# Kernel optimization log

Measured on AMD Instinct MI355X. Metric: run time of the kernel, lower is better.

The kernel has to match this reference:

```python
import jax, jax.numpy as jnp
import numpy as np

TEMPERATURE = 1.0
MAX_ITERS = 10
EPSILON = 1e-4
N, D, K = 131072, 64, 64


def setup_inputs() -> dict:
    key = jax.random.key(0)
    k1, k2 = jax.random.split(key)
    weights = jax.random.normal(k1, (N, D), dtype=jnp.float32)
    init_clusters = jax.random.normal(k2, (K, D), dtype=jnp.float32)
    return {"weights": weights, "init_clusters": init_clusters}


def _dkm(weights, init_clusters):
    n, d = weights.shape
    k = init_clusters.shape[0]
    w_sq = jnp.sum(weights * weights, axis=1, keepdims=True)  # [N,1]

    def step(carry, _):
        clusters, attn_prev, done = carry
        # Euclidean cdist via the expansion ||w||^2 + ||c||^2 - 2 w.c
        c_sq = jnp.sum(clusters * clusters, axis=1)               # [K]
        d2 = w_sq + c_sq[None, :] - 2.0 * (weights @ clusters.T)  # [N,K]
        dist = jnp.sqrt(jnp.maximum(d2, 0.0))
        attn = jax.nn.softmax(-dist / TEMPERATURE, axis=-1)        # [N,K]
        new_clusters = (attn.T @ weights) / jnp.sum(attn, axis=0)[:, None]  # [K,D]
        converged = jnp.linalg.norm(clusters - new_clusters) <= EPSILON
        # Torch breaks BEFORE assigning new_clusters; emulate with a done flag.
        clusters_next = jnp.where(done | converged, clusters, new_clusters)
        attn_next = jnp.where(done, attn_prev, attn)
        return (clusters_next, attn_next, done | converged), None

    init = (init_clusters, jnp.zeros((n, k), weights.dtype), jnp.array(False))
    (clusters, attn, _), _ = jax.lax.scan(step, init, None, length=MAX_ITERS)
    compressed = attn @ clusters  # [N,D]
    return compressed, clusters, attn


def reference(weights, init_clusters):
    return _dkm(weights, init_clusters)
```

## Files before the change

kernel.cpp:

```cpp
#include <hip/hip_runtime.h>
#include <math.h>
#include <stdint.h>

#define N_ROWS 131072
#define DIM 64
#define KC 64
#define NBLK 1024
#define ROWS_PB 128

typedef __attribute__((ext_vector_type(8))) short short8;
typedef __attribute__((ext_vector_type(8))) unsigned short ushort8;
typedef __attribute__((ext_vector_type(16))) float float16;
typedef __attribute__((ext_vector_type(4))) unsigned int uint4v;
typedef __attribute__((ext_vector_type(2))) unsigned long long ulong2v;

#define PARTIAL_OFF 0u
#define SUMA_OFF    4194304u
#define NEWC_OFF    4259840u
#define NORM_BYTE_OFF (4263936ull * 4ull)

__device__ __forceinline__ uint32_t rne16(float a) {
  uint32_t u = __float_as_uint(a);
  return (u + 0x7fffu + ((u >> 16) & 1u)) >> 16;
}

__device__ __forceinline__ uint32_t pack_bf16(float a, float b) {
  return rne16(a) | (rne16(b) << 16);
}

__device__ __forceinline__ void split2(float a, float b, uint32_t& hi, uint32_t& lo) {
  uint32_t ha = rne16(a), hb = rne16(b);
  hi = ha | (hb << 16);
  float la = a - __uint_as_float(ha << 16);
  float lb = b - __uint_as_float(hb << 16);
  lo = pack_bf16(la, lb);
}

__global__ __launch_bounds__(256, 3) void dkm_iter(
    const float* __restrict__ W, const float* __restrict__ Cinit,
    const float* __restrict__ newC, float* __restrict__ cur,
    const double* __restrict__ normpart,
    float* __restrict__ partial, float* __restrict__ sumA,
    float* __restrict__ attn_out, int useSel, int writeAttn)
{
  __shared__ __align__(16) short CbfHi[64][68];
  __shared__ __align__(16) short CbfLo[64][68];
  __shared__ __align__(16) short attnT[64][136];
  __shared__ __align__(16) short WTsh[64][136];
  __shared__ float csqL[64];
  __shared__ float wsqL[128];
  __shared__ int s_cond;

  const int t = threadIdx.x;
  const int blk = blockIdx.x;
  const int wid = t >> 6, lane = t & 63, l31 = lane & 31, lh = lane >> 5;
  const int mg = wid >> 1, ng = wid & 1;
  const int chunkBase = blk * ROWS_PB;
  const int myrow = chunkBase + wid * 32 + l31;
  const int colA = wid * 32 + l31;

  if (wid == 0) {
    double v = 0.0;
    if (useSel) {
#pragma unroll
      for (int i = 0; i < 8; ++i) v += normpart[lane + 64 * i];
    }
    v += __shfl_xor(v, 1); v += __shfl_xor(v, 2); v += __shfl_xor(v, 4);
    v += __shfl_xor(v, 8); v += __shfl_xor(v, 16); v += __shfl_xor(v, 32);
    if (lane == 0) s_cond = (v > 1.0e-8) ? 1 : 0;
  }
  __syncthreads();

  const float* src = useSel ? (s_cond ? newC : cur) : Cinit;

  {
    const int crow = t >> 2, cc = (t & 3) * 16;
    float sq = 0.f;
#pragma unroll
    for (int q = 0; q < 4; ++q) {
      float4 c0 = *(const float4*)(src + crow * 64 + cc + q * 4);
      if (blk == 0) *(float4*)(cur + crow * 64 + cc + q * 4) = c0;
      uint32_t h0, h1, l0, l1;
      split2(c0.x, c0.y, h0, l0);
      split2(c0.z, c0.w, h1, l1);
      uint32_t* ph = (uint32_t*)&CbfHi[crow][cc + q * 4];
      ph[0] = h0; ph[1] = h1;
      uint32_t* pl = (uint32_t*)&CbfLo[crow][cc + q * 4];
      pl[0] = l0; pl[1] = l1;
      sq += c0.x*c0.x + c0.y*c0.y + c0.z*c0.z + c0.w*c0.w;
    }
    sq += __shfl_xor(sq, 1);
    sq += __shfl_xor(sq, 2);
    if ((t & 3) == 0) csqL[crow] = sq;
  }
  __syncthreads();

  float16 dot0 = {0,0,0,0, 0,0,0,0, 0,0,0,0, 0,0,0,0};
  float16 dot1 = {0,0,0,0, 0,0,0,0, 0,0,0,0, 0,0,0,0};
  float w2acc = 0.f;
  const float* pw = W + (size_t)myrow * 64 + lh * 8;
#pragma unroll
  for (int ko = 0; ko < 4; ++ko) {
    float4 a = *(const float4*)(pw + ko * 16);
    float4 b = *(const float4*)(pw + ko * 16 + 4);
    w2acc += a.x*a.x + a.y*a.y + a.z*a.z + a.w*a.w
           + b.x*b.x + b.y*b.y + b.z*b.z + b.w*b.w;
    uint32_t h0, h1, h2, h3, l0, l1, l2, l3;
    split2(a.x, a.y, h0, l0); split2(a.z, a.w, h1, l1);
    split2(b.x, b.y, h2, l2); split2(b.z, b.w, h3, l3);
    const int d0 = ko * 16 + lh * 8;
    WTsh[d0 + 0][colA] = (short)h0;  WTsh[d0 + 1][colA] = (short)(h0 >> 16);
    WTsh[d0 + 2][colA] = (short)h1;  WTsh[d0 + 3][colA] = (short)(h1 >> 16);
    WTsh[d0 + 4][colA] = (short)h2;  WTsh[d0 + 5][colA] = (short)(h2 >> 16);
    WTsh[d0 + 6][colA] = (short)h3;  WTsh[d0 + 7][colA] = (short)(h3 >> 16);
    uint4v th = {h0, h1, h2, h3};
    uint4v tl = {l0, l1, l2, l3};
    short8 aHi = __builtin_bit_cast(short8, th);
    short8 aLo = __builtin_bit_cast(short8, tl);
#pragma unroll
    for (int nt = 0; nt < 2; ++nt) {
      const unsigned long long* ph = (const unsigned long long*)&CbfHi[nt * 32 + l31][ko * 16 + lh * 8];
      const unsigned long long* pl = (const unsigned long long*)&CbfLo[nt * 32 + l31][ko * 16 + lh * 8];
      ulong2v vh = {ph[0], ph[1]};
      ulong2v vl = {pl[0], pl[1]};
      short8 cHi = __builtin_bit_cast(short8, vh);
      short8 cLo = __builtin_bit_cast(short8, vl);
      float16& dd = nt ? dot1 : dot0;
      dd = __builtin_amdgcn_mfma_f32_32x32x16_bf16(aHi, cHi, dd, 0, 0, 0);
      dd = __builtin_amdgcn_mfma_f32_32x32x16_bf16(aLo, cHi, dd, 0, 0, 0);
      dd = __builtin_amdgcn_mfma_f32_32x32x16_bf16(aHi, cLo, dd, 0, 0, 0);
    }
  }
  w2acc += __shfl_xor(w2acc, 32);
  if (lane < 32) wsqL[wid * 32 + l31] = w2acc;

  const float cq0 = csqL[l31], cq1 = csqL[32 + l31];
#pragma unroll
  for (int j = 0; j < 16; ++j) {
    const int trow = (j & 3) + 8 * (j >> 2) + 4 * lh;
    const float w2 = wsqL[wid * 32 + trow];
    float g0 = -sqrtf(fmaxf(fmaf(-2.f, dot0[j], w2 + cq0), 0.f));
    float g1 = -sqrtf(fmaxf(fmaf(-2.f, dot1[j], w2 + cq1), 0.f));
    dot0[j] = __expf(g0);
    dot1[j] = __expf(g1);
  }

  if (writeAttn) {
#pragma unroll
    for (int j = 0; j < 16; ++j) {
      const int trow = (j & 3) + 8 * (j >> 2) + 4 * lh;
      float sj = dot0[j] + dot1[j];
      sj += __shfl_xor(sj, 1);  sj += __shfl_xor(sj, 2);  sj += __shfl_xor(sj, 4);
      sj += __shfl_xor(sj, 8);  sj += __shfl_xor(sj, 16);
      float inv = __builtin_amdgcn_rcpf(sj);
      attn_out[(size_t)(chunkBase + wid * 32 + trow) * 64 + l31] = dot0[j] * inv;
      attn_out[(size_t)(chunkBase + wid * 32 + trow) * 64 + 32 + l31] = dot1[j] * inv;
    }
  }

  {
    uint32_t* aT = (uint32_t*)&attnT[0][0];
    const int cb = wid * 16;
#pragma unroll
    for (int h = 0; h < 4; ++h) {
      const int base = cb + 4 * h + 2 * lh;
      aT[l31 * 68 + base]     = pack_bf16(dot0[4 * h],     dot0[4 * h + 1]);
      aT[l31 * 68 + base + 1] = pack_bf16(dot0[4 * h + 2], dot0[4 * h + 3]);
      aT[(32 + l31) * 68 + base]     = pack_bf16(dot1[4 * h],     dot1[4 * h + 1]);
      aT[(32 + l31) * 68 + base + 1] = pack_bf16(dot1[4 * h + 2], dot1[4 * h + 3]);
    }
  }
  __syncthreads();

  float* invsL = wsqL;
  {
    const int r = t >> 1, kh = t & 1;
    float s = 0.f;
#pragma unroll
    for (int kk = 0; kk < 32; ++kk) {
      uint32_t v = (uint32_t)(unsigned short)attnT[kh * 32 + kk][r];
      s += __uint_as_float(v << 16);
    }
    s += __shfl_xor(s, 1);
    if (kh == 0) invsL[r] = __builtin_amdgcn_rcpf(s);
  }
  __syncthreads();

  {
    const int k = t >> 2, q = t & 3;
    uint32_t* row = (uint32_t*)&attnT[k][0];
#pragma unroll
    for (int i = 0; i < 16; ++i) {
      const int r2 = q * 32 + 2 * i;
      uint32_t dv = row[q * 16 + i];
      float lo = __uint_as_float(dv << 16) * invsL[r2];
      float hi = __uint_as_float(dv & 0xffff0000u) * invsL[r2 + 1];
      row[q * 16 + i] = pack_bf16(lo, hi);
    }
  }
  __syncthreads();

  float16 Uacc = {0,0,0,0, 0,0,0,0, 0,0,0,0, 0,0,0,0};
#pragma unroll
  for (int kc = 0; kc < 8; ++kc) {
    const unsigned long long* pa =
        (const unsigned long long*)&attnT[mg * 32 + l31][kc * 16 + lh * 8];
    ulong2v va = {pa[0], pa[1]};
    short8 af = __builtin_bit_cast(short8, va);
    const unsigned long long* pb =
        (const unsigned long long*)&WTsh[ng * 32 + l31][kc * 16 + lh * 8];
    ulong2v vb = {pb[0], pb[1]};
    short8 bf = __builtin_bit_cast(short8, vb);
    Uacc = __builtin_amdgcn_mfma_f32_32x32x16_bf16(af, bf, Uacc, 0, 0, 0);
  }

  float ssum = 0.f;
  {
    const int sk = t & 63, sg = t >> 6;
#pragma unroll
    for (int q2 = 0; q2 < 4; ++q2) {
      const uint32_t* pq = (const uint32_t*)&attnT[sk][sg * 32 + q2 * 8];
#pragma unroll
      for (int w = 0; w < 4; ++w) {
        uint32_t dv = pq[w];
        ssum += __uint_as_float(dv << 16) + __uint_as_float(dv & 0xffff0000u);
      }
    }
  }

#pragma unroll
  for (int j = 0; j < 16; ++j) {
    const int k = mg * 32 + (j & 3) + 8 * (j >> 2) + 4 * lh;
    partial[((size_t)blk * 64 + k) * 64 + ng * 32 + l31] = Uacc[j];
  }

  __syncthreads();
  float* red = (float*)&CbfHi[0][0];
  red[t] = ssum;
  __syncthreads();
  if (t < 64) sumA[blk * 64 + t] = (red[t] + red[t + 64]) + (red[t + 128] + red[t + 192]);
}

__global__ __launch_bounds__(256) void reduce_kernel(
    const float* __restrict__ partial, const float* __restrict__ sumAp,
    const float* __restrict__ curC, float* __restrict__ newC,
    double* __restrict__ normpart) {
  const int k = blockIdx.x >> 3, oct = blockIdx.x & 7;
  const int t = threadIdx.x;
  const int d = oct * 8 + (t & 7), q = t >> 3;
  double acc = 0.0;
  for (int b = q * 32; b < q * 32 + 32; ++b)
    acc += (double)partial[((size_t)b * 64 + k) * 64 + d];
  __shared__ double sh[256];
  __shared__ double sh2[256];
  sh[t] = acc;
  sh2[t] = ((double)sumAp[t * 64 + k] + (double)sumAp[(t + 256) * 64 + k]) +
           ((double)sumAp[(t + 512) * 64 + k] + (double)sumAp[(t + 768) * 64 + k]);
  __syncthreads();
#pragma unroll
  for (int s = 128; s >= 8; s >>= 1) {
    if (t < s) { sh[t] += sh[t + s]; sh2[t] += sh2[t + s]; }
    __syncthreads();
  }
#pragma unroll
  for (int s = 4; s >= 1; s >>= 1) {
    if (t < s) sh2[t] += sh2[t + s];
    __syncthreads();
  }
  if (t < 8) {
    float nc = (float)(sh[t] / sh2[0]);
    newC[k * 64 + d] = nc;
    double diff = (double)curC[k * 64 + d] - (double)nc;
    sh[t] = diff * diff;
  }
  __syncthreads();
  if (t == 0) {
    double s = 0.0;
#pragma unroll
    for (int i = 0; i < 8; ++i) s += sh[i];
    normpart[blockIdx.x] = s;
  }
}

__global__ __launch_bounds__(256) void finalize_kernel(
    const double* __restrict__ np, const float* __restrict__ newC,
    const float* __restrict__ cur, float* __restrict__ clusters_out) {
  __shared__ double sh[64];
  __shared__ int sc;
  int t = threadIdx.x;
  if (t < 64) {
    double v = 0.0;
#pragma unroll
    for (int i = 0; i < 8; ++i) v += np[t + 64 * i];
    sh[t] = v;
  }
  __syncthreads();
  if (t == 0) {
    double s = 0.0;
    for (int i = 0; i < 64; ++i) s += sh[i];
    sc = (s > 1.0e-8) ? 1 : 0;
  }
  __syncthreads();
  const float* src = sc ? newC : cur;
  for (int m = t; m < 4096; m += 256) {
    float v = src[m];
    clusters_out[m] = v;
  }
}

__global__ __launch_bounds__(256) void compress_kernel(
    const float* __restrict__ attn, const float* __restrict__ Cl,
    float* __restrict__ outC) {
  __shared__ float Csh[64 * 64];
  __shared__ float Ash[64 * 64];
  float4* Csh4 = (float4*)Csh;
  float4* Ash4 = (float4*)Ash;
  const int t = threadIdx.x;
  const int blk = blockIdx.x;
  const int rowBase = blk * 256;
  const int rg = t >> 4, dg = t & 15;

  {
    const float4* gC = (const float4*)Cl;
#pragma unroll
    for (int q = 0; q < 4; ++q) {
      int m = t + 256 * q;
      Csh4[m ^ ((m >> 6) & 15)] = gC[m];
    }
  }

  for (int tile = 0; tile < 4; ++tile) {
    __syncthreads();
    {
      const float4* gA = (const float4*)(attn + (size_t)(rowBase + tile * 64) * KC);
#pragma unroll
      for (int q = 0; q < 4; ++q) {
        int m = t + 256 * q;
        Ash4[m ^ ((m >> 6) & 15)] = gA[m];
      }
    }
    __syncthreads();
    float acc[4][4] = {{0.f}};
#pragma unroll 4
    for (int c = 0; c < 16; ++c) {
      float4 av[4], cv[4];
#pragma unroll
      for (int i = 0; i < 4; ++i) av[i] = Ash4[((rg * 4 + i) * 16 + c) ^ rg];
#pragma unroll
      for (int j = 0; j < 4; ++j) cv[j] = Csh4[((c * 4 + j) * 16 + dg) ^ c];
#pragma unroll
      for (int i = 0; i < 4; ++i) {
        float a0 = fmaf(av[i].x, cv[0].x, acc[i][0]);
        a0 = fmaf(av[i].y, cv[1].x, a0);
        a0 = fmaf(av[i].z, cv[2].x, a0);
        acc[i][0] = fmaf(av[i].w, cv[3].x, a0);
        float a1 = fmaf(av[i].x, cv[0].y, acc[i][1]);
        a1 = fmaf(av[i].y, cv[1].y, a1);
        a1 = fmaf(av[i].z, cv[2].y, a1);
        acc[i][1] = fmaf(av[i].w, cv[3].y, a1);
        float a2 = fmaf(av[i].x, cv[0].z, acc[i][2]);
        a2 = fmaf(av[i].y, cv[1].z, a2);
        a2 = fmaf(av[i].z, cv[2].z, a2);
        acc[i][2] = fmaf(av[i].w, cv[3].z, a2);
        float a3 = fmaf(av[i].x, cv[0].w, acc[i][3]);
        a3 = fmaf(av[i].y, cv[1].w, a3);
        a3 = fmaf(av[i].z, cv[2].w, a3);
        acc[i][3] = fmaf(av[i].w, cv[3].w, a3);
      }
    }
    float4* gO = (float4*)(outC + (size_t)(rowBase + tile * 64) * DIM);
#pragma unroll
    for (int i = 0; i < 4; ++i)
      gO[(rg * 4 + i) * 16 + dg] = make_float4(acc[i][0], acc[i][1], acc[i][2], acc[i][3]);
  }
}

extern "C" void kernel_launch(void* const* d_in, const int* in_sizes, int n_in,
                              void* d_out, int out_size, void* d_ws, size_t ws_size,
                              hipStream_t stream) {
  (void)in_sizes; (void)n_in; (void)d_ws; (void)ws_size; (void)out_size;
  const float* W = (const float*)d_in[0];
  const float* Cinit = (const float*)d_in[1];
  float* ob = (float*)d_out;

  float* compressed = ob;
  float* clusters_out = ob + (size_t)N_ROWS * DIM;
  float* attn_out = ob + (size_t)N_ROWS * DIM + KC * DIM;

  float* partial = ob + PARTIAL_OFF;
  float* sumAp = ob + SUMA_OFF;
  float* newC = ob + NEWC_OFF;
  float* cur = clusters_out;
  double* normpart = (double*)((char*)d_out + NORM_BYTE_OFF);

  for (int it = 0; it < 10; ++it) {
    dkm_iter<<<NBLK, 256, 0, stream>>>(W, Cinit, newC, cur, normpart,
                                       partial, sumAp, attn_out,
                                       (it > 0) ? 1 : 0, (it == 9) ? 1 : 0);
    reduce_kernel<<<512, 256, 0, stream>>>(partial, sumAp, cur, newC, normpart);
  }
  finalize_kernel<<<1, 256, 0, stream>>>(normpart, newC, cur, clusters_out);
  compress_kernel<<<512, 256, 0, stream>>>(attn_out, clusters_out, compressed);
}
```

Baseline: 375.6 us.

## Process two row chunks per block with register prefetch of next chunk's weights

Each block now handles 256 rows as two 128-row chunks, halving the block count and the per-block centroid setup and partial outputs. The weights for the second chunk are loaded into registers during the first chunk's distance/softmax work, so global loads overlap compute. The reduce kernel reads half as many partials, and the LDS normalisation loop staggers its index by row to reduce bank conflicts. The cost is higher register pressure from the prefetched float4 array and fewer blocks to fill the GPU (512 blocks).

```diff
diff --git a/kernel.cpp b/kernel.cpp
--- a/kernel.cpp
+++ b/kernel.cpp
@@ -5,8 +5,8 @@
 #define N_ROWS 131072
 #define DIM 64
 #define KC 64
-#define NBLK 1024
-#define ROWS_PB 128
+#define NBLK 512
+#define ROWS_PB 256
 
 typedef __attribute__((ext_vector_type(8))) short short8;
 typedef __attribute__((ext_vector_type(8))) unsigned short ushort8;
@@ -15,9 +15,9 @@
 typedef __attribute__((ext_vector_type(2))) unsigned long long ulong2v;
 
 #define PARTIAL_OFF 0u
-#define SUMA_OFF    4194304u
-#define NEWC_OFF    4259840u
-#define NORM_BYTE_OFF (4263936ull * 4ull)
+#define SUMA_OFF    2097152u
+#define NEWC_OFF    2129920u
+#define NORM_BYTE_OFF (2134016ull * 4ull)
 
 __device__ __forceinline__ uint32_t rne16(float a) {
   uint32_t u = __float_as_uint(a);
@@ -55,9 +55,14 @@
   const int blk = blockIdx.x;
   const int wid = t >> 6, lane = t & 63, l31 = lane & 31, lh = lane >> 5;
   const int mg = wid >> 1, ng = wid & 1;
-  const int chunkBase = blk * ROWS_PB;
-  const int myrow = chunkBase + wid * 32 + l31;
+  const int rowBase = blk * ROWS_PB;
   const int colA = wid * 32 + l31;
+
+  const float* pwBase = W + (size_t)(rowBase + wid * 32 + l31) * 64 + lh * 8;
+  float4 vv[8];
+#pragma unroll
+  for (int q = 0; q < 8; ++q)
+    vv[q] = *(const float4*)(pwBase + (q >> 1) * 16 + (q & 1) * 4);
 
   if (wid == 0) {
     double v = 0.0;
@@ -95,137 +100,151 @@
   }
   __syncthreads();
 
-  float16 dot0 = {0,0,0,0, 0,0,0,0, 0,0,0,0, 0,0,0,0};
-  float16 dot1 = {0,0,0,0, 0,0,0,0, 0,0,0,0, 0,0,0,0};
-  float w2acc = 0.f;
-  const float* pw = W + (size_t)myrow * 64 + lh * 8;
-#pragma unroll
-  for (int ko = 0; ko < 4; ++ko) {
-    float4 a = *(const float4*)(pw + ko * 16);
-    float4 b = *(const float4*)(pw + ko * 16 + 4);
-    w2acc += a.x*a.x + a.y*a.y + a.z*a.z + a.w*a.w
-           + b.x*b.x + b.y*b.y + b.z*b.z + b.w*b.w;
-    uint32_t h0, h1, h2, h3, l0, l1, l2, l3;
-    split2(a.x, a.y, h0, l0); split2(a.z, a.w, h1, l1);
-    split2(b.x, b.y, h2, l2); split2(b.z, b.w, h3, l3);
-    const int d0 = ko * 16 + lh * 8;
-    WTsh[d0 + 0][colA] = (short)h0;  WTsh[d0 + 1][colA] = (short)(h0 >> 16);
-    WTsh[d0 + 2][colA] = (short)h1;  WTsh[d0 + 3][colA] = (short)(h1 >> 16);
-    WTsh[d0 + 4][colA] = (short)h2;  WTsh[d0 + 5][colA] = (short)(h2 >> 16);
-    WTsh[d0 + 6][colA] = (short)h3;  WTsh[d0 + 7][colA] = (short)(h3 >> 16);
-    uint4v th = {h0, h1, h2, h3};
-    uint4v tl = {l0, l1, l2, l3};
-    short8 aHi = __builtin_bit_cast(short8, th);
-    short8 aLo = __builtin_bit_cast(short8, tl);
-#pragma unroll
-    for (int nt = 0; nt < 2; ++nt) {
-      const unsigned long long* ph = (const unsigned long long*)&CbfHi[nt * 32 + l31][ko * 16 + lh * 8];
-      const unsigned long long* pl = (const unsigned long long*)&CbfLo[nt * 32 + l31][ko * 16 + lh * 8];
-      ulong2v vh = {ph[0], ph[1]};
-      ulong2v vl = {pl[0], pl[1]};
-      short8 cHi = __builtin_bit_cast(short8, vh);
-      short8 cLo = __builtin_bit_cast(short8, vl);
-      float16& dd = nt ? dot1 : dot0;
-      dd = __builtin_amdgcn_mfma_f32_32x32x16_bf16(aHi, cHi, dd, 0, 0, 0);
-      dd = __builtin_amdgcn_mfma_f32_32x32x16_bf16(aLo, cHi, dd, 0, 0, 0);
-      dd = __builtin_amdgcn_mfma_f32_32x32x16_bf16(aHi, cLo, dd, 0, 0, 0);
-    }
-  }
-  w2acc += __shfl_xor(w2acc, 32);
-  if (lane < 32) wsqL[wid * 32 + l31] = w2acc;
-
+  float16 Uacc = {0,0,0,0, 0,0,0,0, 0,0,0,0, 0,0,0,0};
+  float ssumAll = 0.f;
   const float cq0 = csqL[l31], cq1 = csqL[32 + l31];
-#pragma unroll
-  for (int j = 0; j < 16; ++j) {
-    const int trow = (j & 3) + 8 * (j >> 2) + 4 * lh;
-    const float w2 = wsqL[wid * 32 + trow];
-    float g0 = -sqrtf(fmaxf(fmaf(-2.f, dot0[j], w2 + cq0), 0.f));
-    float g1 = -sqrtf(fmaxf(fmaf(-2.f, dot1[j], w2 + cq1), 0.f));
-    dot0[j] = __expf(g0);
-    dot1[j] = __expf(g1);
-  }
-
-  if (writeAttn) {
+
+#pragma unroll
+  for (int c = 0; c < 2; ++c) {
+    const int chunkBase = rowBase + c * 128;
+
+    float16 dot0 = {0,0,0,0, 0,0,0,0, 0,0,0,0, 0,0,0,0};
+    float16 dot1 = {0,0,0,0, 0,0,0,0, 0,0,0,0, 0,0,0,0};
+    float w2acc = 0.f;
+#pragma unroll
+    for (int ko = 0; ko < 4; ++ko) {
+      float4 a = vv[ko * 2];
+      float4 b = vv[ko * 2 + 1];
+      w2acc += a.x*a.x + a.y*a.y + a.z*a.z + a.w*a.w
+             + b.x*b.x + b.y*b.y + b.z*b.z + b.w*b.w;
+      uint32_t h0, h1, h2, h3, l0, l1, l2, l3;
+      split2(a.x, a.y, h0, l0); split2(a.z, a.w, h1, l1);
+      split2(b.x, b.y, h2, l2); split2(b.z, b.w, h3, l3);
+      const int d0 = ko * 16 + lh * 8;
+      WTsh[d0 + 0][colA] = (short)h0;  WTsh[d0 + 1][colA] = (short)(h0 >> 16);
+      WTsh[d0 + 2][colA] = (short)h1;  WTsh[d0 + 3][colA] = (short)(h1 >> 16);
+      WTsh[d0 + 4][colA] = (short)h2;  WTsh[d0 + 5][colA] = (short)(h2 >> 16);
+      WTsh[d0 + 6][colA] = (short)h3;  WTsh[d0 + 7][colA] = (short)(h3 >> 16);
+      uint4v th = {h0, h1, h2, h3};
+      uint4v tl = {l0, l1, l2, l3};
+      short8 aHi = __builtin_bit_cast(short8, th);
+      short8 aLo = __builtin_bit_cast(short8, tl);
+#pragma unroll
+      for (int nt = 0; nt < 2; ++nt) {
+        const unsigned long long* ph = (const unsigned long long*)&CbfHi[nt * 32 + l31][ko * 16 + lh * 8];
+        const unsigned long long* pl = (const unsigned long long*)&CbfLo[nt * 32 + l31][ko * 16 + lh * 8];
+        ulong2v vh = {ph[0], ph[1]};
+        ulong2v vl = {pl[0], pl[1]};
+        short8 cHi = __builtin_bit_cast(short8, vh);
+        short8 cLo = __builtin_bit_cast(short8, vl);
+        float16& dd = nt ? dot1 : dot0;
+        dd = __builtin_amdgcn_mfma_f32_32x32x16_bf16(aHi, cHi, dd, 0, 0, 0);
+        dd = __builtin_amdgcn_mfma_f32_32x32x16_bf16(aLo, cHi, dd, 0, 0, 0);
+        dd = __builtin_amdgcn_mfma_f32_32x32x16_bf16(aHi, cLo, dd, 0, 0, 0);
+      }
+    }
+    w2acc += __shfl_xor(w2acc, 32);
+    if (lane < 32) wsqL[wid * 32 + l31] = w2acc;
+
+    if (c == 0) {
+      const float* pwN = pwBase + 128 * 64;
+#pragma unroll
+      for (int q = 0; q < 8; ++q)
+        vv[q] = *(const float4*)(pwN + (q >> 1) * 16 + (q & 1) * 4);
+    }
+
 #pragma unroll
     for (int j = 0; j < 16; ++j) {
       const int trow = (j & 3) + 8 * (j >> 2) + 4 * lh;
-      float sj = dot0[j] + dot1[j];
-      sj += __shfl_xor(sj, 1);  sj += __shfl_xor(sj, 2);  sj += __shfl_xor(sj, 4);
-      sj += __shfl_xor(sj, 8);  sj += __shfl_xor(sj, 16);
-      float inv = __builtin_amdgcn_rcpf(sj);
-      attn_out[(size_t)(chunkBase + wid * 32 + trow) * 64 + l31] = dot0[j] * inv;
-      attn_out[(size_t)(chunkBase + wid * 32 + trow) * 64 + 32 + l31] = dot1[j] * inv;
-    }
-  }
-
-  {
-    uint32_t* aT = (uint32_t*)&attnT[0][0];
-    const int cb = wid * 16;
-#pragma unroll
-    for (int h = 0; h < 4; ++h) {
-      const int base = cb + 4 * h + 2 * lh;
-      aT[l31 * 68 + base]     = pack_bf16(dot0[4 * h],     dot0[4 * h + 1]);
-      aT[l31 * 68 + base + 1] = pack_bf16(dot0[4 * h + 2], dot0[4 * h + 3]);
-      aT[(32 + l31) * 68 + base]     = pack_bf16(dot1[4 * h],     dot1[4 * h + 1]);
-      aT[(32 + l31) * 68 + base + 1] = pack_bf16(dot1[4 * h + 2], dot1[4 * h + 3]);
-    }
-  }
-  __syncthreads();
-
-  float* invsL = wsqL;
-  {
-    const int r = t >> 1, kh = t & 1;
-    float s = 0.f;
-#pragma unroll
-    for (int kk = 0; kk < 32; ++kk) {
-      uint32_t v = (uint32_t)(unsigned short)attnT[kh * 32 + kk][r];
-      s += __uint_as_float(v << 16);
-    }
-    s += __shfl_xor(s, 1);
-    if (kh == 0) invsL[r] = __builtin_amdgcn_rcpf(s);
-  }
-  __syncthreads();
-
-  {
-    const int k = t >> 2, q = t & 3;
-    uint32_t* row = (uint32_t*)&attnT[k][0];
-#pragma unroll
-    for (int i = 0; i < 16; ++i) {
-      const int r2 = q * 32 + 2 * i;
-      uint32_t dv = row[q * 16 + i];
-      float lo = __uint_as_float(dv << 16) * invsL[r2];
-      float hi = __uint_as_float(dv & 0xffff0000u) * invsL[r2 + 1];
-      row[q * 16 + i] = pack_bf16(lo, hi);
-    }
-  }
-  __syncthreads();
-
-  float16 Uacc = {0,0,0,0, 0,0,0,0, 0,0,0,0, 0,0,0,0};
-#pragma unroll
-  for (int kc = 0; kc < 8; ++kc) {
-    const unsigned long long* pa =
-        (const unsigned long long*)&attnT[mg * 32 + l31][kc * 16 + lh * 8];
-    ulong2v va = {pa[0], pa[1]};
-    short8 af = __builtin_bit_cast(short8, va);
-    const unsigned long long* pb =
-        (const unsigned long long*)&WTsh[ng * 32 + l31][kc * 16 + lh * 8];
-    ulong2v vb = {pb[0], pb[1]};
-    short8 bf = __builtin_bit_cast(short8, vb);
-    Uacc = __builtin_amdgcn_mfma_f32_32x32x16_bf16(af, bf, Uacc, 0, 0, 0);
-  }
-
-  float ssum = 0.f;
-  {
-    const int sk = t & 63, sg = t >> 6;
-#pragma unroll
-    for (int q2 = 0; q2 < 4; ++q2) {
-      const uint32_t* pq = (const uint32_t*)&attnT[sk][sg * 32 + q2 * 8];
-#pragma unroll
-      for (int w = 0; w < 4; ++w) {
-        uint32_t dv = pq[w];
-        ssum += __uint_as_float(dv << 16) + __uint_as_float(dv & 0xffff0000u);
-      }
-    }
+      const float w2 = wsqL[wid * 32 + trow];
+      float g0 = -sqrtf(fmaxf(fmaf(-2.f, dot0[j], w2 + cq0), 0.f));
+      float g1 = -sqrtf(fmaxf(fmaf(-2.f, dot1[j], w2 + cq1), 0.f));
+      dot0[j] = __expf(g0);
+      dot1[j] = __expf(g1);
+    }
+
+    if (writeAttn) {
+#pragma unroll
+      for (int j = 0; j < 16; ++j) {
+        const int trow = (j & 3) + 8 * (j >> 2) + 4 * lh;
+        float sj = dot0[j] + dot1[j];
+        sj += __shfl_xor(sj, 1);  sj += __shfl_xor(sj, 2);  sj += __shfl_xor(sj, 4);
+        sj += __shfl_xor(sj, 8);  sj += __shfl_xor(sj, 16);
+        float inv = __builtin_amdgcn_rcpf(sj);
+        attn_out[(size_t)(chunkBase + wid * 32 + trow) * 64 + l31] = dot0[j] * inv;
+        attn_out[(size_t)(chunkBase + wid * 32 + trow) * 64 + 32 + l31] = dot1[j] * inv;
+      }
+    }
+
+    {
+      uint32_t* aT = (uint32_t*)&attnT[0][0];
+      const int cb = wid * 16;
+#pragma unroll
+      for (int h = 0; h < 4; ++h) {
+        const int base = cb + 4 * h + 2 * lh;
+        aT[l31 * 68 + base]     = pack_bf16(dot0[4 * h],     dot0[4 * h + 1]);
+        aT[l31 * 68 + base + 1] = pack_bf16(dot0[4 * h + 2], dot0[4 * h + 3]);
+        aT[(32 + l31) * 68 + base]     = pack_bf16(dot1[4 * h],     dot1[4 * h + 1]);
+        aT[(32 + l31) * 68 + base + 1] = pack_bf16(dot1[4 * h + 2], dot1[4 * h + 3]);
+      }
+    }
+    __syncthreads();
+
+    float* invsL = wsqL;
+    {
+      const int r = t >> 1, kh = t & 1;
+      float s = 0.f;
+#pragma unroll
+      for (int kk = 0; kk < 32; ++kk) {
+        uint32_t v = (uint32_t)(unsigned short)attnT[kh * 32 + kk][r];
+        s += __uint_as_float(v << 16);
+      }
+      s += __shfl_xor(s, 1);
+      if (kh == 0) invsL[r] = __builtin_amdgcn_rcpf(s);
+    }
+    __syncthreads();
+
+    {
+      const int k = t >> 2, q = t & 3;
+      uint32_t* row = (uint32_t*)&attnT[k][0];
+#pragma unroll
+      for (int i = 0; i < 16; ++i) {
+        const int ii = (i + k) & 15;
+        const int r2 = q * 32 + 2 * ii;
+        uint32_t dv = row[q * 16 + ii];
+        float lo = __uint_as_float(dv << 16) * invsL[r2];
+        float hi = __uint_as_float(dv & 0xffff0000u) * invsL[r2 + 1];
+        row[q * 16 + ii] = pack_bf16(lo, hi);
+      }
+    }
+    __syncthreads();
+
+#pragma unroll
+    for (int kc = 0; kc < 8; ++kc) {
+      const unsigned long long* pa =
+          (const unsigned long long*)&attnT[mg * 32 + l31][kc * 16 + lh * 8];
+      ulong2v va = {pa[0], pa[1]};
+      short8 af = __builtin_bit_cast(short8, va);
+      const unsigned long long* pb =
+          (const unsigned long long*)&WTsh[ng * 32 + l31][kc * 16 + lh * 8];
+      ulong2v vb = {pb[0], pb[1]};
+      short8 bf = __builtin_bit_cast(short8, vb);
+      Uacc = __builtin_amdgcn_mfma_f32_32x32x16_bf16(af, bf, Uacc, 0, 0, 0);
+    }
+
+    {
+      const int sk = t & 63, sg = t >> 6;
+#pragma unroll
+      for (int q2 = 0; q2 < 4; ++q2) {
+        const uint32_t* pq = (const uint32_t*)&attnT[sk][sg * 32 + q2 * 8];
+#pragma unroll
+        for (int w = 0; w < 4; ++w) {
+          uint32_t dv = pq[w];
+          ssumAll += __uint_as_float(dv << 16) + __uint_as_float(dv & 0xffff0000u);
+        }
+      }
+    }
+    __syncthreads();
   }
 
 #pragma unroll
@@ -234,9 +253,8 @@
     partial[((size_t)blk * 64 + k) * 64 + ng * 32 + l31] = Uacc[j];
   }
 
-  __syncthreads();
   float* red = (float*)&CbfHi[0][0];
-  red[t] = ssum;
+  red[t] = ssumAll;
   __syncthreads();
   if (t < 64) sumA[blk * 64 + t] = (red[t] + red[t + 64]) + (red[t + 128] + red[t + 192]);
 }
@@ -249,13 +267,12 @@
   const int t = threadIdx.x;
   const int d = oct * 8 + (t & 7), q = t >> 3;
   double acc = 0.0;
-  for (int b = q * 32; b < q * 32 + 32; ++b)
+  for (int b = q * 16; b < q * 16 + 16; ++b)
     acc += (double)partial[((size_t)b * 64 + k) * 64 + d];
   __shared__ double sh[256];
   __shared__ double sh2[256];
   sh[t] = acc;
-  sh2[t] = ((double)sumAp[t * 64 + k] + (double)sumAp[(t + 256) * 64 + k]) +
-           ((double)sumAp[(t + 512) * 64 + k] + (double)sumAp[(t + 768) * 64 + k]);
+  sh2[t] = (double)sumAp[t * 64 + k] + (double)sumAp[(t + 256) * 64 + k];
   __syncthreads();
 #pragma unroll
   for (int s = 128; s >= 8; s >>= 1) {
```

Measured after the change: 354.8 us. 1.06x faster.

## Prefetch weights early, remap block order, compute attention sums via MFMA

Applied to the files above, without the earlier changes.

Weight-row loads for each thread are issued at kernel start, before the convergence check and cluster staging, so global latency overlaps that setup work. Block indices are permuted so consecutive launched blocks touch strided row chunks, and the LDS normalization loop is rotated per row to reduce bank conflicts. The per-cluster attention column sums are computed with an extra MFMA against a ones vector instead of a scalar LDS reduction plus two barriers. The cost is more registers held across the early phase, which may reduce occupancy.

```diff
diff --git a/kernel.cpp b/kernel.cpp
--- a/kernel.cpp
+++ b/kernel.cpp
@@ -52,12 +52,19 @@
   __shared__ int s_cond;
 
   const int t = threadIdx.x;
-  const int blk = blockIdx.x;
+  const int raw = blockIdx.x;
+  const int blk = ((raw & 7) << 7) | (raw >> 3);
   const int wid = t >> 6, lane = t & 63, l31 = lane & 31, lh = lane >> 5;
   const int mg = wid >> 1, ng = wid & 1;
-  const int chunkBase = blk * ROWS_PB;
-  const int myrow = chunkBase + wid * 32 + l31;
+  const int rowBase = blk * ROWS_PB;
+  const int myrow = rowBase + wid * 32 + l31;
   const int colA = wid * 32 + l31;
+
+  const float* pwBase = W + (size_t)myrow * 64 + lh * 8;
+  float4 vv[8];
+#pragma unroll
+  for (int q = 0; q < 8; ++q)
+    vv[q] = *(const float4*)(pwBase + (q >> 1) * 16 + (q & 1) * 4);
 
   if (wid == 0) {
     double v = 0.0;
@@ -79,7 +86,7 @@
 #pragma unroll
     for (int q = 0; q < 4; ++q) {
       float4 c0 = *(const float4*)(src + crow * 64 + cc + q * 4);
-      if (blk == 0) *(float4*)(cur + crow * 64 + cc + q * 4) = c0;
+      if (raw == 0) *(float4*)(cur + crow * 64 + cc + q * 4) = c0;
       uint32_t h0, h1, l0, l1;
       split2(c0.x, c0.y, h0, l0);
       split2(c0.z, c0.w, h1, l1);
@@ -98,11 +105,10 @@
   float16 dot0 = {0,0,0,0, 0,0,0,0, 0,0,0,0, 0,0,0,0};
   float16 dot1 = {0,0,0,0, 0,0,0,0, 0,0,0,0, 0,0,0,0};
   float w2acc = 0.f;
-  const float* pw = W + (size_t)myrow * 64 + lh * 8;
 #pragma unroll
   for (int ko = 0; ko < 4; ++ko) {
-    float4 a = *(const float4*)(pw + ko * 16);
-    float4 b = *(const float4*)(pw + ko * 16 + 4);
+    float4 a = vv[ko * 2];
+    float4 b = vv[ko * 2 + 1];
     w2acc += a.x*a.x + a.y*a.y + a.z*a.z + a.w*a.w
            + b.x*b.x + b.y*b.y + b.z*b.z + b.w*b.w;
     uint32_t h0, h1, h2, h3, l0, l1, l2, l3;
@@ -153,8 +159,8 @@
       sj += __shfl_xor(sj, 1);  sj += __shfl_xor(sj, 2);  sj += __shfl_xor(sj, 4);
       sj += __shfl_xor(sj, 8);  sj += __shfl_xor(sj, 16);
       float inv = __builtin_amdgcn_rcpf(sj);
-      attn_out[(size_t)(chunkBase + wid * 32 + trow) * 64 + l31] = dot0[j] * inv;
-      attn_out[(size_t)(chunkBase + wid * 32 + trow) * 64 + 32 + l31] = dot1[j] * inv;
+      attn_out[(size_t)(rowBase + wid * 32 + trow) * 64 + l31] = dot0[j] * inv;
+      attn_out[(size_t)(rowBase + wid * 32 + trow) * 64 + 32 + l31] = dot1[j] * inv;
     }
   }
 
@@ -191,16 +197,20 @@
     uint32_t* row = (uint32_t*)&attnT[k][0];
 #pragma unroll
     for (int i = 0; i < 16; ++i) {
-      const int r2 = q * 32 + 2 * i;
-      uint32_t dv = row[q * 16 + i];
+      const int ii = (i + k) & 15;
+      const int r2 = q * 32 + 2 * ii;
+      uint32_t dv = row[q * 16 + ii];
       float lo = __uint_as_float(dv << 16) * invsL[r2];
       float hi = __uint_as_float(dv & 0xffff0000u) * invsL[r2 + 1];
-      row[q * 16 + i] = pack_bf16(lo, hi);
+      row[q * 16 + ii] = pack_bf16(lo, hi);
     }
   }
   __syncthreads();
 
   float16 Uacc = {0,0,0,0, 0,0,0,0, 0,0,0,0, 0,0,0,0};
+  float16 Uacc1 = {0,0,0,0, 0,0,0,0, 0,0,0,0, 0,0,0,0};
+  const short8 ones = {0x3F80, 0x3F80, 0x3F80, 0x3F80,
+                       0x3F80, 0x3F80, 0x3F80, 0x3F80};
 #pragma unroll
   for (int kc = 0; kc < 8; ++kc) {
     const unsigned long long* pa =
@@ -212,20 +222,7 @@
     ulong2v vb = {pb[0], pb[1]};
     short8 bf = __builtin_bit_cast(short8, vb);
     Uacc = __builtin_amdgcn_mfma_f32_32x32x16_bf16(af, bf, Uacc, 0, 0, 0);
-  }
-
-  float ssum = 0.f;
-  {
-    const int sk = t & 63, sg = t >> 6;
-#pragma unroll
-    for (int q2 = 0; q2 < 4; ++q2) {
-      const uint32_t* pq = (const uint32_t*)&attnT[sk][sg * 32 + q2 * 8];
-#pragma unroll
-      for (int w = 0; w < 4; ++w) {
-        uint32_t dv = pq[w];
-        ssum += __uint_as_float(dv << 16) + __uint_as_float(dv & 0xffff0000u);
-      }
-    }
+    Uacc1 = __builtin_amdgcn_mfma_f32_32x32x16_bf16(af, ones, Uacc1, 0, 0, 0);
   }
 
 #pragma unroll
@@ -233,12 +230,13 @@
     const int k = mg * 32 + (j & 3) + 8 * (j >> 2) + 4 * lh;
     partial[((size_t)blk * 64 + k) * 64 + ng * 32 + l31] = Uacc[j];
   }
-
-  __syncthreads();
-  float* red = (float*)&CbfHi[0][0];
-  red[t] = ssum;
-  __syncthreads();
-  if (t < 64) sumA[blk * 64 + t] = (red[t] + red[t + 64]) + (red[t + 128] + red[t + 192]);
+  if (ng == 0 && l31 == 0) {
+#pragma unroll
+    for (int j = 0; j < 16; ++j) {
+      const int k = mg * 32 + (j & 3) + 8 * (j >> 2) + 4 * lh;
+      sumA[blk * 64 + k] = Uacc1[j];
+    }
+  }
 }
 
 __global__ __launch_bounds__(256) void reduce_kernel(
```

Result: slower. 389.3 us (+3.7%).
